# Performance work log

Hardware: AMD Instinct MI355X
Metric: run time of the kernel (lower is better)

The kernel has to match this reference:

```python
import jax, jax.numpy as jnp
import numpy as np
import math

D_MODEL = 256
PRED_LEN = 256
K = 32
LOW_FREQ = 1


def setup_inputs() -> dict:
    key = jax.random.key(0)
    x = jax.random.normal(key, (8, 1024, D_MODEL), dtype=jnp.float32)
    return {"x": x}


def reference(x):
    """x: (b, t, d) -> reconstructed/extrapolated series (b, t+pred_len, d)."""
    b, t, d = x.shape
    k_ = K  # K < t//2, so the explicit-k branch of the torch module is taken

    x_freq = jnp.fft.rfft(x, axis=1)  # (b, t//2+1, d) complex
    if t % 2 == 0:
        x_freq_high = x_freq[:, LOW_FREQ:-1]  # drop DC..low_freq-1 and Nyquist
    else:
        x_freq_high = x_freq[:, LOW_FREQ:]

    # top-k magnitudes over the frequency axis, independently per (b, d)
    mag = jnp.abs(x_freq_high)                                   # (b, F, d)
    _, idx = jax.lax.top_k(jnp.transpose(mag, (0, 2, 1)), k_)    # (b, d, k)
    idx = jnp.transpose(idx, (0, 2, 1)) + LOW_FREQ               # (b, k, d) into x_freq

    x_freq_topk = jnp.take_along_axis(x_freq, idx, axis=1)       # (b, k, d) complex
    freqs = jnp.fft.rfftfreq(t).astype(x.dtype)                  # (t//2+1,)
    f_topk = freqs[idx]                                          # (b, k, d)

    # append conjugate / negative-frequency pair for a real reconstruction
    x_ext = jnp.concatenate([x_freq_topk, jnp.conj(x_freq_topk)], axis=1)  # (b, 2k, d)
    f_ext = jnp.concatenate([f_topk, -f_topk], axis=1)                     # (b, 2k, d)

    t_val = jnp.arange(t + PRED_LEN, dtype=x.dtype)              # (T,)
    amp = (jnp.abs(x_ext) / t)[:, :, None, :]                    # (b, 2k, 1, d)
    phase = jnp.angle(x_ext)[:, :, None, :]                      # (b, 2k, 1, d)
    arg = (2.0 * math.pi) * f_ext[:, :, None, :] * t_val[None, None, :, None] + phase
    x_time = amp * jnp.cos(arg)                                  # (b, 2k, T, d)
    return jnp.sum(x_time, axis=1)                               # (b, T, d)
```

## Files before the change

### kernel.cpp

```cpp
#include <hip/hip_runtime.h>
#include <math.h>

#define T_LEN 1024
#define PRED_LEN 256
#define OUT_T (T_LEN + PRED_LEN)
#define DM 256
#define KSEL 32

#define TWO_PI_F 6.2831853071795864769f
#define INV1024  0.0009765625f

#define SPAD(i) ((i) + ((i) >> 5))

#define C1_ 0.92387953251128675613
#define C2_ 0.70710678118654752440
#define C3_ 0.38268343236508977173
__device__ __constant__ double W16R_[16] = {
    1.0,  C1_,  C2_,  C3_, 0.0, -C3_, -C2_, -C1_,
   -1.0, -C1_, -C2_, -C3_, 0.0,  C3_,  C2_,  C1_ };
__device__ __constant__ double W16I_[16] = {
    0.0, -C3_, -C2_, -C1_, -1.0, -C1_, -C2_, -C3_,
    0.0,  C3_,  C2_,  C1_,  1.0,  C1_,  C2_,  C3_ };

#define R2_ 0.70710678118654752440f
__device__ __constant__ float CW8[8] = { 1.0f,  R2_, 0.0f, -R2_, -1.0f, -R2_,  0.0f,  R2_ };
__device__ __constant__ float SW8[8] = { 0.0f,  R2_, 1.0f,  R2_,  0.0f, -R2_, -1.0f, -R2_ };

__global__ void fl_twiddle_kernel(double* __restrict__ gwr, double* __restrict__ gwi) {
    int e = blockIdx.x * 64 + threadIdx.x;
    double ang = (double)e * (6.283185307179586476925286766559 / 1024.0);
    gwr[e] = cos(ang);
    gwi[e] = -sin(ang);
}

__global__ void __launch_bounds__(256, 4)
fl_fused_kernel(const float* __restrict__ x,
                const double* __restrict__ gwr, const double* __restrict__ gwi,
                float* __restrict__ out) {
    __shared__ double reS[SPAD(1023) + 1], imS[SPAD(1023) + 1];
    __shared__ char smemA[8192];
    __shared__ int hist[512];
    __shared__ int   selMs[2 * KSEL];
    __shared__ float selAs[2 * KSEL], selBs[2 * KSEL];
    float2* xsh = (float2*)smemA;
    double* mg  = (double*)smemA;

    const int tid  = threadIdx.x;
    const int lane = tid & 63;
    const int w    = tid >> 6;

    const int bid = blockIdx.x;
    const int sp  = ((bid & 7) << 7) | (bid >> 3);
    const int b   = sp >> 7;
    const int d0  = (sp & 127) << 1;

    for (int j = 0; j < 4; ++j) {
        int e = tid + (j << 8);
        reS[SPAD(e)] = gwr[e];
        imS[SPAD(e)] = gwi[e];
        xsh[e] = *reinterpret_cast<const float2*>(&x[(((size_t)(b << 10) + e) << 8) + d0]);
    }
    __syncthreads();

    double ar[4], ai[4];
#pragma unroll
    for (int pass = 0; pass < 2; ++pass) {
        double Sr[2][4], Si[2][4];
#pragma unroll
        for (int qq = 0; qq < 2; ++qq)
#pragma unroll
            for (int n1a = 0; n1a < 4; ++n1a) { Sr[qq][n1a] = 0.0; Si[qq][n1a] = 0.0; }
#pragma unroll
        for (int n1b = 0; n1b < 4; ++n1b) {
#pragma unroll
            for (int n1a = 0; n1a < 4; ++n1a) {
                float2 xv = xsh[lane + 64 * (n1a + 4 * n1b)];
                double xr = (double)xv.x, xi = (double)xv.y;
#pragma unroll
                for (int qq = 0; qq < 2; ++qq) {
                    const int q = pass * 2 + qq;
                    const int r = (n1b * q) & 3;
                    if      (r == 0) { Sr[qq][n1a] += xr; Si[qq][n1a] += xi; }
                    else if (r == 1) { Sr[qq][n1a] += xi; Si[qq][n1a] -= xr; }
                    else if (r == 2) { Sr[qq][n1a] -= xr; Si[qq][n1a] -= xi; }
                    else             { Sr[qq][n1a] -= xi; Si[qq][n1a] += xr; }
                }
            }
        }
#pragma unroll
        for (int qq = 0; qq < 2; ++qq) {
            const int q  = pass * 2 + qq;
            const int k1 = (w << 2) | q;
            double cr = Sr[qq][0], ci = Si[qq][0];
#pragma unroll
            for (int n1a = 1; n1a < 4; ++n1a) {
                int e = (n1a * k1) & 15;
                double wr = W16R_[e], wi = W16I_[e];
                cr += Sr[qq][n1a] * wr - Si[qq][n1a] * wi;
                ci += Sr[qq][n1a] * wi + Si[qq][n1a] * wr;
            }
            int et = (lane * k1) & 1023;
            double twr = reS[SPAD(et)], twi = imS[SPAD(et)];
            ar[q] = cr * twr - ci * twi;
            ai[q] = cr * twi + ci * twr;
        }
    }

#pragma unroll
    for (int s = 0; s < 6; ++s) {
        const int half = 32 >> s;
        const int e = (lane & (half - 1)) << s;
        const double wr = reS[SPAD(e << 4)];
        const double wi = imS[SPAD(e << 4)];
        const bool up = (lane & half) != 0;
#pragma unroll
        for (int q = 0; q < 4; ++q) {
            double orr = __shfl_xor(ar[q], half);
            double oii = __shfl_xor(ai[q], half);
            double sr = ar[q] + orr, si = ai[q] + oii;
            double dr = orr - ar[q], di = oii - ai[q];
            double ur = dr * wr - di * wi;
            double ui = dr * wi + di * wr;
            ar[q] = up ? ur : sr;
            ai[q] = up ? ui : si;
        }
    }
    __syncthreads();

    {
        const int krev = (int)(__brev((unsigned)lane) >> 26);
#pragma unroll
        for (int q = 0; q < 4; ++q) {
            int k = ((w << 2) | q) + (krev << 4);
            reS[SPAD(k)] = ar[q];
            imS[SPAD(k)] = ai[q];
        }
    }
    __syncthreads();

#pragma unroll
    for (int h = 0; h < 2; ++h) {
        int m = tid + (h << 8);
        int n = (1024 - m) & 1023;
        double rm = reS[SPAD(m)], iv = imS[SPAD(m)];
        double rn = reS[SPAD(n)], in_ = imS[SPAD(n)];
        double rr0 = 0.5 * (rm + rn),  ii0 = 0.5 * (iv - in_);
        double rr1 = 0.5 * (iv + in_), ii1 = 0.5 * (rn - rm);
        mg[m]       = rr0 * rr0 + ii0 * ii0;
        mg[512 + m] = rr1 * rr1 + ii1 * ii1;
    }
    __syncthreads();

    if (tid < 128) {
        const int c = tid >> 6;
        const double* mgc = mg + (c << 9);
        int* histc = hist + (c << 8);

        double v[8]; int hiw[8];
#pragma unroll
        for (int q = 0; q < 8; ++q) v[q] = mgc[(q << 6) | lane];
        if (lane == 0) v[0] = -1.0;
#pragma unroll
        for (int q = 0; q < 8; ++q) hiw[q] = __double2hiint(v[q]);

        int mx = hiw[0];
#pragma unroll
        for (int q = 1; q < 8; ++q) mx = max(mx, hiw[q]);
#pragma unroll
        for (int off = 1; off < 64; off <<= 1) mx = max(mx, __shfl_xor(mx, off));

        const int base = (mx >> 17) - 250;
        int idx[8];
#pragma unroll
        for (int q = 0; q < 8; ++q) {
            int t = (hiw[q] >> 17) - base;
            idx[q] = t < 0 ? 0 : t;
        }

        *reinterpret_cast<int4*>(&histc[lane << 2]) = int4{0, 0, 0, 0};
#pragma unroll
        for (int q = 0; q < 8; ++q) atomicAdd(&histc[idx[q]], 1);

        int4 cc = *reinterpret_cast<int4*>(&histc[lane << 2]);
        int s_local = cc.x + cc.y + cc.z + cc.w;

        int s = s_local;
#pragma unroll
        for (int off = 1; off < 64; off <<= 1) {
            int t = __shfl_down(s, off);
            if (lane + off < 64) s += t;
        }
        const int S_gt = s - s_local;
        const int A3 = S_gt;
        const int A2 = A3 + cc.w;
        const int A1 = A2 + cc.z;
        const int A0 = A1 + cc.y;

        int foundB = -1, foundR = 0;
        if (A0 < KSEL && A0 + cc.x >= KSEL) { foundB = (lane << 2) | 0; foundR = KSEL - A0; }
        if (A1 < KSEL && A1 + cc.y >= KSEL) { foundB = (lane << 2) | 1; foundR = KSEL - A1; }
        if (A2 < KSEL && A2 + cc.z >= KSEL) { foundB = (lane << 2) | 2; foundR = KSEL - A2; }
        if (A3 < KSEL && A3 + cc.w >= KSEL) { foundB = (lane << 2) | 3; foundR = KSEL - A3; }

        unsigned long long fm = __ballot(foundB >= 0);
        const int src = (int)(__ffsll((unsigned long long)fm) - 1);
        const int B = __shfl(foundB, src);
        const int r = __shfl(foundR, src);

        unsigned selmask = 0, candmask = 0;
#pragma unroll
        for (int q = 0; q < 8; ++q) {
            if (idx[q] > B) selmask |= (1u << q);
            else if (idx[q] == B) candmask |= (1u << q);
        }

        for (int it = 0; it < r; ++it) {
            double bv = -2.0; int bq = -1;
#pragma unroll
            for (int q = 0; q < 8; ++q) {
                bool cand = ((candmask >> q) & 1u) != 0;
                if (cand && v[q] > bv) { bv = v[q]; bq = q; }
            }
            int bi = (bq < 0) ? 0x7FFFFFFF : ((bq << 6) | lane);
#pragma unroll
            for (int off = 1; off < 64; off <<= 1) {
                double ov = __shfl_xor(bv, off);
                int    oi = __shfl_xor(bi, off);
                if (ov > bv || (ov == bv && oi < bi)) { bv = ov; bi = oi; }
            }
            if (bi != 0x7FFFFFFF && lane == (bi & 63)) {
                unsigned bit = 1u << (bi >> 6);
                selmask  |= bit;
                candmask &= ~bit;
            }
        }

        const int cnt = __popc(selmask);
        int p = cnt;
#pragma unroll
        for (int off = 1; off < 64; off <<= 1) {
            int t = __shfl_up(p, off);
            if (lane >= off) p += t;
        }
        int slot = (c << 5) + (p - cnt);

#pragma unroll
        for (int q = 0; q < 8; ++q) {
            if ((selmask >> q) & 1u) {
                int m = (q << 6) | lane;
                int n = (1024 - m) & 1023;
                double rm = reS[SPAD(m)], iv = imS[SPAD(m)];
                double rn = reS[SPAD(n)], in_ = imS[SPAD(n)];
                double rr, ii;
                if (c == 0) { rr = 0.5 * (rm + rn);  ii = 0.5 * (iv - in_); }
                else        { rr = 0.5 * (iv + in_); ii = 0.5 * (rn - rm); }
                selMs[slot] = m;
                selAs[slot] = (float)( rr / 512.0);
                selBs[slot] = (float)(-ii / 512.0);
                ++slot;
            }
        }
    }
    __syncthreads();

    {
        const int col = tid & 1;
        const int j   = tid >> 1;
        float acc[10];
#pragma unroll
        for (int i = 0; i < 10; ++i) acc[i] = 0.0f;

        const int cbase = col << 5;
        for (int k = 0; k < KSEL; ++k) {
            const int   m = selMs[cbase + k];
            const float A = selAs[cbase + k];
            const float B = selBs[cbase + k];
            const int   r = m & 7;
            const float cw = CW8[r], sw = SW8[r];
            const float th = (float)((m * j) & 1023) * (INV1024 * TWO_PI_F);
            float cs = __cosf(th);
            float sn = __sinf(th);
#pragma unroll
            for (int i = 0; i < 10; ++i) {
                acc[i] = fmaf(A, cs, fmaf(B, sn, acc[i]));
                float cn = fmaf(cs, cw, -(sn * sw));
                float s2 = fmaf(sn, cw,  (cs * sw));
                cs = cn; sn = s2;
            }
        }

        float* op = out + ((size_t)b * OUT_T + j) * DM + d0 + col;
#pragma unroll
        for (int i = 0; i < 10; ++i) {
            op[(size_t)i * 128 * DM] = acc[i];
        }
    }
}

extern "C" void kernel_launch(void* const* d_in, const int* in_sizes, int n_in,
                              void* d_out, int out_size, void* d_ws, size_t ws_size,
                              hipStream_t stream) {
    const float* x = (const float*)d_in[0];
    float* out = (float*)d_out;

    char* w = (char*)d_ws;
    double* gwr = (double*)(w);
    double* gwi = (double*)(w + 1024 * sizeof(double));

    hipLaunchKernelGGL(fl_twiddle_kernel, dim3(16), dim3(64), 0, stream, gwr, gwi);
    hipLaunchKernelGGL(fl_fused_kernel, dim3(1024), dim3(256), 0, stream,
                       x, gwr, gwi, out);
}
```

Baseline: 43.99 us.

## Compute FFT and top-k selection in fp32 with fp64 recheck of near-ties

Moves the per-column FFT, butterfly stages, magnitude computation and histogram-based top-k selection from double to single precision, halving shared-memory twiddle storage and avoiding slow fp64 arithmetic. The first-stage radix-4 is also rewritten as explicit butterflies. To keep the selection correct near the k-th boundary, candidates whose magnitudes fall inside a relative window around the threshold are recomputed with a direct fp64 DFT from global twiddles and reselected. This adds a rarely-taken but costly fallback path and a second twiddle table.

```diff
diff --git a/kernel.cpp b/kernel.cpp
--- a/kernel.cpp
+++ b/kernel.cpp
@@ -9,41 +9,41 @@
 
 #define TWO_PI_F 6.2831853071795864769f
 #define INV1024  0.0009765625f
+#define RTAU 1e-4f
 
 #define SPAD(i) ((i) + ((i) >> 5))
 
-#define C1_ 0.92387953251128675613
-#define C2_ 0.70710678118654752440
-#define C3_ 0.38268343236508977173
-__device__ __constant__ double W16R_[16] = {
-    1.0,  C1_,  C2_,  C3_, 0.0, -C3_, -C2_, -C1_,
-   -1.0, -C1_, -C2_, -C3_, 0.0,  C3_,  C2_,  C1_ };
-__device__ __constant__ double W16I_[16] = {
-    0.0, -C3_, -C2_, -C1_, -1.0, -C1_, -C2_, -C3_,
-    0.0,  C3_,  C2_,  C1_,  1.0,  C1_,  C2_,  C3_ };
+__device__ __constant__ float W16RF[16] = {
+    1.0f,  0.92387953f,  0.70710678f,  0.38268343f, 0.0f, -0.38268343f, -0.70710678f, -0.92387953f,
+   -1.0f, -0.92387953f, -0.70710678f, -0.38268343f, 0.0f,  0.38268343f,  0.70710678f,  0.92387953f };
+__device__ __constant__ float W16IF[16] = {
+    0.0f, -0.38268343f, -0.70710678f, -0.92387953f, -1.0f, -0.92387953f, -0.70710678f, -0.38268343f,
+    0.0f,  0.38268343f,  0.70710678f,  0.92387953f,  1.0f,  0.92387953f,  0.70710678f,  0.38268343f };
 
 #define R2_ 0.70710678118654752440f
 __device__ __constant__ float CW8[8] = { 1.0f,  R2_, 0.0f, -R2_, -1.0f, -R2_,  0.0f,  R2_ };
 __device__ __constant__ float SW8[8] = { 0.0f,  R2_, 1.0f,  R2_,  0.0f, -R2_, -1.0f, -R2_ };
 
-__global__ void fl_twiddle_kernel(double* __restrict__ gwr, double* __restrict__ gwi) {
+__global__ void fl_twiddle_kernel(double* __restrict__ gwr, double* __restrict__ gwi,
+                                  float* __restrict__ gwrF, float* __restrict__ gwiF) {
     int e = blockIdx.x * 64 + threadIdx.x;
     double ang = (double)e * (6.283185307179586476925286766559 / 1024.0);
-    gwr[e] = cos(ang);
-    gwi[e] = -sin(ang);
+    double c = cos(ang), s = -sin(ang);
+    gwr[e] = c; gwi[e] = s;
+    gwrF[e] = (float)c; gwiF[e] = (float)s;
 }
 
 __global__ void __launch_bounds__(256, 4)
 fl_fused_kernel(const float* __restrict__ x,
                 const double* __restrict__ gwr, const double* __restrict__ gwi,
+                const float* __restrict__ gwrF, const float* __restrict__ gwiF,
                 float* __restrict__ out) {
-    __shared__ double reS[SPAD(1023) + 1], imS[SPAD(1023) + 1];
-    __shared__ char smemA[8192];
+    __shared__ float gspR[SPAD(1023) + 1], gspI[SPAD(1023) + 1];
+    __shared__ float2 xsh[1024];
+    __shared__ float mg[1024];
     __shared__ int hist[512];
     __shared__ int   selMs[2 * KSEL];
     __shared__ float selAs[2 * KSEL], selBs[2 * KSEL];
-    float2* xsh = (float2*)smemA;
-    double* mg  = (double*)smemA;
 
     const int tid  = threadIdx.x;
     const int lane = tid & 63;
@@ -56,71 +56,62 @@
 
     for (int j = 0; j < 4; ++j) {
         int e = tid + (j << 8);
-        reS[SPAD(e)] = gwr[e];
-        imS[SPAD(e)] = gwi[e];
+        gspR[SPAD(e)] = gwrF[e];
+        gspI[SPAD(e)] = gwiF[e];
         xsh[e] = *reinterpret_cast<const float2*>(&x[(((size_t)(b << 10) + e) << 8) + d0]);
     }
     __syncthreads();
 
-    double ar[4], ai[4];
-#pragma unroll
-    for (int pass = 0; pass < 2; ++pass) {
-        double Sr[2][4], Si[2][4];
-#pragma unroll
-        for (int qq = 0; qq < 2; ++qq)
-#pragma unroll
-            for (int n1a = 0; n1a < 4; ++n1a) { Sr[qq][n1a] = 0.0; Si[qq][n1a] = 0.0; }
-#pragma unroll
-        for (int n1b = 0; n1b < 4; ++n1b) {
-#pragma unroll
-            for (int n1a = 0; n1a < 4; ++n1a) {
-                float2 xv = xsh[lane + 64 * (n1a + 4 * n1b)];
-                double xr = (double)xv.x, xi = (double)xv.y;
-#pragma unroll
-                for (int qq = 0; qq < 2; ++qq) {
-                    const int q = pass * 2 + qq;
-                    const int r = (n1b * q) & 3;
-                    if      (r == 0) { Sr[qq][n1a] += xr; Si[qq][n1a] += xi; }
-                    else if (r == 1) { Sr[qq][n1a] += xi; Si[qq][n1a] -= xr; }
-                    else if (r == 2) { Sr[qq][n1a] -= xr; Si[qq][n1a] -= xi; }
-                    else             { Sr[qq][n1a] -= xi; Si[qq][n1a] += xr; }
-                }
-            }
-        }
-#pragma unroll
-        for (int qq = 0; qq < 2; ++qq) {
-            const int q  = pass * 2 + qq;
-            const int k1 = (w << 2) | q;
-            double cr = Sr[qq][0], ci = Si[qq][0];
-#pragma unroll
-            for (int n1a = 1; n1a < 4; ++n1a) {
-                int e = (n1a * k1) & 15;
-                double wr = W16R_[e], wi = W16I_[e];
-                cr += Sr[qq][n1a] * wr - Si[qq][n1a] * wi;
-                ci += Sr[qq][n1a] * wi + Si[qq][n1a] * wr;
-            }
-            int et = (lane * k1) & 1023;
-            double twr = reS[SPAD(et)], twi = imS[SPAD(et)];
-            ar[q] = cr * twr - ci * twi;
-            ai[q] = cr * twi + ci * twr;
-        }
+    float Fr[4][4], Fi[4][4];
+#pragma unroll
+    for (int n1a = 0; n1a < 4; ++n1a) {
+        float2 a  = xsh[lane + 64 * (n1a + 0)];
+        float2 bb = xsh[lane + 64 * (n1a + 4)];
+        float2 cV = xsh[lane + 64 * (n1a + 8)];
+        float2 d  = xsh[lane + 64 * (n1a + 12)];
+        float t0r = a.x + cV.x, t0i = a.y + cV.y;
+        float t1r = a.x - cV.x, t1i = a.y - cV.y;
+        float t2r = bb.x + d.x, t2i = bb.y + d.y;
+        float t3r = bb.x - d.x, t3i = bb.y - d.y;
+        Fr[n1a][0] = t0r + t2r;  Fi[n1a][0] = t0i + t2i;
+        Fr[n1a][2] = t0r - t2r;  Fi[n1a][2] = t0i - t2i;
+        Fr[n1a][1] = t1r + t3i;  Fi[n1a][1] = t1i - t3r;
+        Fr[n1a][3] = t1r - t3i;  Fi[n1a][3] = t1i + t3r;
+    }
+
+    float ar[4], ai[4];
+#pragma unroll
+    for (int q = 0; q < 4; ++q) {
+        const int k1 = (w << 2) | q;
+        float cr = Fr[0][q], ci = Fi[0][q];
+#pragma unroll
+        for (int n1a = 1; n1a < 4; ++n1a) {
+            int e = (n1a * k1) & 15;
+            float wr = W16RF[e], wi = W16IF[e];
+            cr += Fr[n1a][q] * wr - Fi[n1a][q] * wi;
+            ci += Fr[n1a][q] * wi + Fi[n1a][q] * wr;
+        }
+        int et = (lane * k1) & 1023;
+        float twr = gspR[SPAD(et)], twi = gspI[SPAD(et)];
+        ar[q] = cr * twr - ci * twi;
+        ai[q] = cr * twi + ci * twr;
     }
 
 #pragma unroll
     for (int s = 0; s < 6; ++s) {
         const int half = 32 >> s;
         const int e = (lane & (half - 1)) << s;
-        const double wr = reS[SPAD(e << 4)];
-        const double wi = imS[SPAD(e << 4)];
+        const float wr = gspR[SPAD(e << 4)];
+        const float wi = gspI[SPAD(e << 4)];
         const bool up = (lane & half) != 0;
 #pragma unroll
         for (int q = 0; q < 4; ++q) {
-            double orr = __shfl_xor(ar[q], half);
-            double oii = __shfl_xor(ai[q], half);
-            double sr = ar[q] + orr, si = ai[q] + oii;
-            double dr = orr - ar[q], di = oii - ai[q];
-            double ur = dr * wr - di * wi;
-            double ui = dr * wi + di * wr;
+            float orr = __shfl_xor(ar[q], half);
+            float oii = __shfl_xor(ai[q], half);
+            float sr = ar[q] + orr, si = ai[q] + oii;
+            float dr = orr - ar[q], di = oii - ai[q];
+            float ur = dr * wr - di * wi;
+            float ui = dr * wi + di * wr;
             ar[q] = up ? ur : sr;
             ai[q] = up ? ui : si;
         }
@@ -132,8 +123,8 @@
 #pragma unroll
         for (int q = 0; q < 4; ++q) {
             int k = ((w << 2) | q) + (krev << 4);
-            reS[SPAD(k)] = ar[q];
-            imS[SPAD(k)] = ai[q];
+            gspR[SPAD(k)] = ar[q];
+            gspI[SPAD(k)] = ai[q];
         }
     }
     __syncthreads();
@@ -142,10 +133,10 @@
     for (int h = 0; h < 2; ++h) {
         int m = tid + (h << 8);
         int n = (1024 - m) & 1023;
-        double rm = reS[SPAD(m)], iv = imS[SPAD(m)];
-        double rn = reS[SPAD(n)], in_ = imS[SPAD(n)];
-        double rr0 = 0.5 * (rm + rn),  ii0 = 0.5 * (iv - in_);
-        double rr1 = 0.5 * (iv + in_), ii1 = 0.5 * (rn - rm);
+        float rm = gspR[SPAD(m)], iv = gspI[SPAD(m)];
+        float rn = gspR[SPAD(n)], in_ = gspI[SPAD(n)];
+        float rr0 = 0.5f * (rm + rn),  ii0 = 0.5f * (iv - in_);
+        float rr1 = 0.5f * (iv + in_), ii1 = 0.5f * (rn - rm);
         mg[m]       = rr0 * rr0 + ii0 * ii0;
         mg[512 + m] = rr1 * rr1 + ii1 * ii1;
     }
@@ -153,15 +144,15 @@
 
     if (tid < 128) {
         const int c = tid >> 6;
-        const double* mgc = mg + (c << 9);
+        const float* mgc = mg + (c << 9);
         int* histc = hist + (c << 8);
 
-        double v[8]; int hiw[8];
+        float v[8]; int hiw[8];
 #pragma unroll
         for (int q = 0; q < 8; ++q) v[q] = mgc[(q << 6) | lane];
-        if (lane == 0) v[0] = -1.0;
-#pragma unroll
-        for (int q = 0; q < 8; ++q) hiw[q] = __double2hiint(v[q]);
+        if (lane == 0) v[0] = -1.0f;
+#pragma unroll
+        for (int q = 0; q < 8; ++q) hiw[q] = __float_as_int(v[q]);
 
         int mx = hiw[0];
 #pragma unroll
@@ -169,11 +160,11 @@
 #pragma unroll
         for (int off = 1; off < 64; off <<= 1) mx = max(mx, __shfl_xor(mx, off));
 
-        const int base = (mx >> 17) - 250;
+        const int base = (mx >> 20) - 250;
         int idx[8];
 #pragma unroll
         for (int q = 0; q < 8; ++q) {
-            int t = (hiw[q] >> 17) - base;
+            int t = (hiw[q] >> 20) - base;
             idx[q] = t < 0 ? 0 : t;
         }
 
@@ -203,9 +194,9 @@
         if (A3 < KSEL && A3 + cc.w >= KSEL) { foundB = (lane << 2) | 3; foundR = KSEL - A3; }
 
         unsigned long long fm = __ballot(foundB >= 0);
-        const int src = (int)(__ffsll((unsigned long long)fm) - 1);
-        const int B = __shfl(foundB, src);
-        const int r = __shfl(foundR, src);
+        const int srcB = (int)(__ffsll((unsigned long long)fm) - 1);
+        const int B = __shfl(foundB, srcB);
+        const int r = __shfl(foundR, srcB);
 
         unsigned selmask = 0, candmask = 0;
 #pragma unroll
@@ -215,7 +206,7 @@
         }
 
         for (int it = 0; it < r; ++it) {
-            double bv = -2.0; int bq = -1;
+            float bv = -2.0f; int bq = -1;
 #pragma unroll
             for (int q = 0; q < 8; ++q) {
                 bool cand = ((candmask >> q) & 1u) != 0;
@@ -224,8 +215,8 @@
             int bi = (bq < 0) ? 0x7FFFFFFF : ((bq << 6) | lane);
 #pragma unroll
             for (int off = 1; off < 64; off <<= 1) {
-                double ov = __shfl_xor(bv, off);
-                int    oi = __shfl_xor(bi, off);
+                float ov = __shfl_xor(bv, off);
+                int   oi = __shfl_xor(bi, off);
                 if (ov > bv || (ov == bv && oi < bi)) { bv = ov; bi = oi; }
             }
             if (bi != 0x7FFFFFFF && lane == (bi & 63)) {
@@ -235,6 +226,75 @@
             }
         }
 
+        {
+            float vminS = 3.0e38f, vmaxU = -3.0e38f;
+#pragma unroll
+            for (int q = 0; q < 8; ++q) {
+                if ((selmask >> q) & 1u) vminS = fminf(vminS, v[q]);
+                else                     vmaxU = fmaxf(vmaxU, v[q]);
+            }
+#pragma unroll
+            for (int off = 1; off < 64; off <<= 1) {
+                vminS = fminf(vminS, __shfl_xor(vminS, off));
+                vmaxU = fmaxf(vmaxU, __shfl_xor(vmaxU, off));
+            }
+            const float tau = RTAU * vminS;
+            if (vminS - vmaxU < tau) {
+                const float lo = vmaxU - tau, hi = vminS + tau;
+                unsigned candq = 0; int nAbove = 0;
+#pragma unroll
+                for (int q = 0; q < 8; ++q) {
+                    bool inw = (v[q] >= lo) && (v[q] <= hi);
+                    if (inw) candq |= (1u << q);
+                    if (((selmask >> q) & 1u) && v[q] > hi) ++nAbove;
+                }
+#pragma unroll
+                for (int off = 1; off < 64; off <<= 1) nAbove += __shfl_xor(nAbove, off);
+                const int kneed = KSEL - nAbove;
+                selmask &= ~candq;
+
+                double sV = -1.0; int sSrc = 0; int cnum = 0;
+                for (int q = 0; q < 8; ++q) {
+                    unsigned long long bal = __ballot((candq >> q) & 1u);
+                    while (bal) {
+                        int srcl = (int)(__ffsll(bal) - 1);
+                        bal &= bal - 1;
+                        int m = (q << 6) | srcl;
+                        double sr = 0.0, si = 0.0;
+                        for (int u = 0; u < 16; ++u) {
+                            int n = lane + (u << 6);
+                            float2 xv2 = xsh[n];
+                            double xvd = (double)(c ? xv2.y : xv2.x);
+                            int e = (m * n) & 1023;
+                            sr = fma(xvd, gwr[e], sr);
+                            si = fma(xvd, gwi[e], si);
+                        }
+#pragma unroll
+                        for (int off = 1; off < 64; off <<= 1) {
+                            sr += __shfl_xor(sr, off);
+                            si += __shfl_xor(si, off);
+                        }
+                        if (lane == cnum) { sV = sr * sr + si * si; sSrc = (q << 6) | srcl; }
+                        ++cnum;
+                        if (cnum >= 64) break;
+                    }
+                    if (cnum >= 64) break;
+                }
+                for (int it = 0; it < kneed; ++it) {
+                    double bv = sV; int bl = lane;
+#pragma unroll
+                    for (int off = 1; off < 64; off <<= 1) {
+                        double ov = __shfl_xor(bv, off);
+                        int    ol = __shfl_xor(bl, off);
+                        if (ov > bv || (ov == bv && ol < bl)) { bv = ov; bl = ol; }
+                    }
+                    int wsrc = __shfl(sSrc, bl);
+                    if (lane == (wsrc & 63)) selmask |= 1u << (wsrc >> 6);
+                    if (lane == bl) sV = -2.0;
+                }
+            }
+        }
+
         const int cnt = __popc(selmask);
         int p = cnt;
 #pragma unroll
@@ -249,14 +309,14 @@
             if ((selmask >> q) & 1u) {
                 int m = (q << 6) | lane;
                 int n = (1024 - m) & 1023;
-                double rm = reS[SPAD(m)], iv = imS[SPAD(m)];
-                double rn = reS[SPAD(n)], in_ = imS[SPAD(n)];
-                double rr, ii;
-                if (c == 0) { rr = 0.5 * (rm + rn);  ii = 0.5 * (iv - in_); }
-                else        { rr = 0.5 * (iv + in_); ii = 0.5 * (rn - rm); }
+                float rm = gspR[SPAD(m)], iv = gspI[SPAD(m)];
+                float rn = gspR[SPAD(n)], in_ = gspI[SPAD(n)];
+                float rr, ii;
+                if (c == 0) { rr = 0.5f * (rm + rn);  ii = 0.5f * (iv - in_); }
+                else        { rr = 0.5f * (iv + in_); ii = 0.5f * (rn - rm); }
                 selMs[slot] = m;
-                selAs[slot] = (float)( rr / 512.0);
-                selBs[slot] = (float)(-ii / 512.0);
+                selAs[slot] = rr * (1.0f / 512.0f);
+                selBs[slot] = -ii * (1.0f / 512.0f);
                 ++slot;
             }
         }
@@ -275,8 +335,8 @@
             const int   m = selMs[cbase + k];
             const float A = selAs[cbase + k];
             const float B = selBs[cbase + k];
-            const int   r = m & 7;
-            const float cw = CW8[r], sw = SW8[r];
+            const int   rr8 = m & 7;
+            const float cw = CW8[rr8], sw = SW8[rr8];
             const float th = (float)((m * j) & 1023) * (INV1024 * TWO_PI_F);
             float cs = __cosf(th);
             float sn = __sinf(th);
@@ -304,10 +364,12 @@
     float* out = (float*)d_out;
 
     char* w = (char*)d_ws;
-    double* gwr = (double*)(w);
-    double* gwi = (double*)(w + 1024 * sizeof(double));
-
-    hipLaunchKernelGGL(fl_twiddle_kernel, dim3(16), dim3(64), 0, stream, gwr, gwi);
+    double* gwr  = (double*)(w);
+    double* gwi  = (double*)(w + 1024 * sizeof(double));
+    float*  gwrF = (float*)(w + 2048 * sizeof(double));
+    float*  gwiF = (float*)(w + 2048 * sizeof(double) + 1024 * sizeof(float));
+
+    hipLaunchKernelGGL(fl_twiddle_kernel, dim3(16), dim3(64), 0, stream, gwr, gwi, gwrF, gwiF);
     hipLaunchKernelGGL(fl_fused_kernel, dim3(1024), dim3(256), 0, stream,
-                       x, gwr, gwi, out);
+                       x, gwr, gwi, gwrF, gwiF, out);
 }
```

New measurement: 41.82 us. 1.05x faster.
